# Kernel tuning notes

Hardware: AMD Instinct MI355X
Metric: run time of the kernel (lower is better)

Reference implementation:

```python
import jax, jax.numpy as jnp
import numpy as np

C_IN, K_R, K_C, N_K = 32, 3, 3, 64
STRIDE = (1, 1)
PAD = (1, 1)


def setup_inputs() -> dict:
    key = jax.random.key(0)
    k1, k2, k3 = jax.random.split(key, 3)
    x = jax.random.normal(k1, (32, C_IN, 128, 128), dtype=jnp.float32)
    kernels = jax.random.normal(k2, (N_K, K_R * K_C * C_IN), dtype=jnp.float32) * 0.05
    bias = jax.random.normal(k3, (N_K, 1), dtype=jnp.float32) * 0.05
    return {"x": x, "kernels": kernels, "bias": bias}


def reference(x, kernels, bias):
    # kernels rows are [C, kr, kc] flattened (per-channel im2col blocks stacked
    # along dim 0 in the original unroll) -> OIHW conv weight.
    w = kernels.reshape(N_K, C_IN, K_R, K_C)
    out = jax.lax.conv_general_dilated(
        x, w,
        window_strides=STRIDE,
        padding=[(PAD[0], PAD[0]), (PAD[1], PAD[1])],
        dimension_numbers=("NCHW", "OIHW", "NCHW"),
    )
    # bias (K, 1) broadcast over all output positions
    return out + bias.reshape(1, N_K, 1, 1)
```

## Files before the change

kernel.cpp:

```cpp
#include <hip/hip_runtime.h>
#include <hip/hip_bf16.h>


typedef __attribute__((ext_vector_type(8))) short bf16x8;
typedef __attribute__((ext_vector_type(4))) float f32x4;

#define NB 32
#define CIN 32
#define HH 128
#define WW 128
#define NK 64
#define XROW (130 * 32)

__device__ __forceinline__ unsigned short f2bf(float f) {
    union { float f; unsigned int u; } v; v.f = f;
    unsigned int u = v.u;
    return (unsigned short)((u + 0x7FFFu + ((u >> 16) & 1u)) >> 16);
}

__device__ __forceinline__ int xel(int wi, int c) {
    return wi * 32 + ((((c >> 3) ^ ((wi >> 2) & 3)) << 3) | (c & 7));
}

__global__ void repack_w(const float* __restrict__ kern,
                         unsigned short* __restrict__ wfrag) {
    int u = blockIdx.x * 256 + threadIdx.x;
    int j = u & 7;
    int lane = (u >> 3) & 63;
    int tile = (u >> 9) & 3;
    int kidx = u >> 11;
    int ok = tile * 16 + (lane & 15);
    int c = ((lane >> 4) << 3) + j;
    wfrag[u] = f2bf(kern[ok * 288 + c * 9 + kidx]);
}

__global__ __launch_bounds__(256, 4) void conv3x3_mfma(
        const float* __restrict__ x, const unsigned short* __restrict__ wfrag,
        const float* __restrict__ bias, float* __restrict__ out) {
    __shared__ unsigned short lds_x[3 * XROW];

    const int tid = threadIdx.x;
    const int bx = blockIdx.x;
    const int h = ((bx & 7) << 4) | (bx >> 3);
    const int n = blockIdx.y;
    const int lane = tid & 63;
    const int l16 = lane & 15;
    const int q = lane >> 4;
    const int wav = tid >> 6;
    const int ok_tile = (wav & 1) * 2;
    const int w_base = (wav >> 1) * 64;

    if (tid < 192) {
        int kr = tid >> 6;
        int idx = tid & 63;
        int c = idx & 31;
        int wi = (idx < 32) ? 0 : 129;
        lds_x[kr * XROW + xel(wi, c)] = 0;
    }

    #pragma unroll
    for (int kr = 0; kr < 3; ++kr) {
        const int r = h + kr - 1;
        const bool valid = (unsigned)r < HH;
        const float* xrow = x + ((size_t)(n * CIN) * HH + r) * WW;
        unsigned short* lrow = lds_x + kr * XROW;
        #pragma unroll
        for (int it = 0; it < 2; ++it) {
            int u = it * 256 + tid;
            int c = (u >> 5) * 2;
            int wq = u & 31;
            float4 va = {0.f, 0.f, 0.f, 0.f}, vb = {0.f, 0.f, 0.f, 0.f};
            if (valid) {
                va = *((const float4*)(xrow + (size_t)c * HH * WW) + wq);
                vb = *((const float4*)(xrow + (size_t)(c + 1) * HH * WW) + wq);
            }
            #pragma unroll
            for (int j = 0; j < 4; ++j) {
                int w = wq * 4 + j;
                __hip_bfloat162 h2 = __float22bfloat162_rn(
                    make_float2((&va.x)[j], (&vb.x)[j]));
                *(unsigned int*)&lrow[xel(w + 1, c)] = *(unsigned int*)&h2;
            }
        }
    }
    __syncthreads();

    f32x4 acc[2][4];
    #pragma unroll
    for (int mi = 0; mi < 2; ++mi)
        #pragma unroll
        for (int ni = 0; ni < 4; ++ni)
            acc[mi][ni] = (f32x4){0.f, 0.f, 0.f, 0.f};

    #pragma unroll 1
    for (int kr = 0; kr < 3; ++kr) {
        const unsigned short* lrow = lds_x + kr * XROW;
        #pragma unroll
        for (int kc = 0; kc < 3; ++kc) {
            const int kidx = kr * 3 + kc;
            bf16x8 afr[2];
            #pragma unroll
            for (int mi = 0; mi < 2; ++mi)
                afr[mi] = *(const bf16x8*)
                    &wfrag[(size_t)(((kidx * 4) + ok_tile + mi) * 64 + lane) * 8];
            #pragma unroll
            for (int ni = 0; ni < 4; ++ni) {
                bf16x8 bfr = *(const bf16x8*)&lrow[xel(w_base + ni * 16 + l16 + kc, q * 8)];
                #pragma unroll
                for (int mi = 0; mi < 2; ++mi)
                    acc[mi][ni] = __builtin_amdgcn_mfma_f32_16x16x32_bf16(
                        afr[mi], bfr, acc[mi][ni], 0, 0, 0);
            }
        }
    }

    #pragma unroll
    for (int mi = 0; mi < 2; ++mi) {
        #pragma unroll
        for (int rg = 0; rg < 4; ++rg) {
            int ok = (wav & 1) * 32 + mi * 16 + q * 4 + rg;
            float bv = bias[ok];
            float* orow = out + ((size_t)(n * NK + ok) * HH + h) * WW;
            #pragma unroll
            for (int ni = 0; ni < 4; ++ni)
                orow[w_base + ni * 16 + l16] = acc[mi][ni][rg] + bv;
        }
    }
}

extern "C" void kernel_launch(void* const* d_in, const int* in_sizes, int n_in,
                              void* d_out, int out_size, void* d_ws, size_t ws_size,
                              hipStream_t stream) {
    const float* x    = (const float*)d_in[0];
    const float* kern = (const float*)d_in[1];
    const float* bias = (const float*)d_in[2];
    float* out = (float*)d_out;
    unsigned short* wfrag = (unsigned short*)d_ws;

    repack_w<<<72, 256, 0, stream>>>(kern, wfrag);
    dim3 grid(HH, NB);
    conv3x3_mfma<<<grid, 256, 0, stream>>>(x, wfrag, bias, out);
}
```

Baseline: 197.7 us.

## Compute two output rows per block sharing a four-row LDS input tile

```diff
diff --git a/kernel.cpp b/kernel.cpp
--- a/kernel.cpp
+++ b/kernel.cpp
@@ -34,46 +34,47 @@
     wfrag[u] = f2bf(kern[ok * 288 + c * 9 + kidx]);
 }
 
-__global__ __launch_bounds__(256, 4) void conv3x3_mfma(
+__global__ __launch_bounds__(512, 6) void conv3x3_mfma(
         const float* __restrict__ x, const unsigned short* __restrict__ wfrag,
         const float* __restrict__ bias, float* __restrict__ out) {
-    __shared__ unsigned short lds_x[3 * XROW];
+    __shared__ unsigned short lds_x[4 * XROW];
 
     const int tid = threadIdx.x;
     const int bx = blockIdx.x;
-    const int h = ((bx & 7) << 4) | (bx >> 3);
+    const int hp = ((bx & 7) << 3) | (bx >> 3);
+    const int h0 = hp * 2;
     const int n = blockIdx.y;
     const int lane = tid & 63;
     const int l16 = lane & 15;
     const int q = lane >> 4;
     const int wav = tid >> 6;
-    const int ok_tile = (wav & 1) * 2;
-    const int w_base = (wav >> 1) * 64;
+    const int hsel = wav >> 2;
+    const int sub = wav & 3;
+    const int ok_tile = (sub & 1) * 2;
+    const int w_base = (sub >> 1) * 64;
 
-    if (tid < 192) {
-        int kr = tid >> 6;
+    if (tid < 256) {
+        int it = tid >> 6;
         int idx = tid & 63;
         int c = idx & 31;
         int wi = (idx < 32) ? 0 : 129;
-        lds_x[kr * XROW + xel(wi, c)] = 0;
+        lds_x[it * XROW + xel(wi, c)] = 0;
     }
 
-    #pragma unroll
-    for (int kr = 0; kr < 3; ++kr) {
-        const int r = h + kr - 1;
-        const bool valid = (unsigned)r < HH;
-        const float* xrow = x + ((size_t)(n * CIN) * HH + r) * WW;
-        unsigned short* lrow = lds_x + kr * XROW;
+    {
+        const int c = (tid >> 5) * 2;
+        const int wq = tid & 31;
         #pragma unroll
-        for (int it = 0; it < 2; ++it) {
-            int u = it * 256 + tid;
-            int c = (u >> 5) * 2;
-            int wq = u & 31;
+        for (int it = 0; it < 4; ++it) {
+            const int r = h0 - 1 + it;
+            const bool valid = (unsigned)r < HH;
             float4 va = {0.f, 0.f, 0.f, 0.f}, vb = {0.f, 0.f, 0.f, 0.f};
             if (valid) {
-                va = *((const float4*)(xrow + (size_t)c * HH * WW) + wq);
-                vb = *((const float4*)(xrow + (size_t)(c + 1) * HH * WW) + wq);
+                const float* xrow = x + (((size_t)n * CIN + c) * HH + r) * WW;
+                va = *((const float4*)xrow + wq);
+                vb = *((const float4*)(xrow + (size_t)HH * WW) + wq);
             }
+            unsigned short* lrow = lds_x + it * XROW;
             #pragma unroll
             for (int j = 0; j < 4; ++j) {
                 int w = wq * 4 + j;
@@ -94,7 +95,7 @@
 
     #pragma unroll 1
     for (int kr = 0; kr < 3; ++kr) {
-        const unsigned short* lrow = lds_x + kr * XROW;
+        const unsigned short* lrow = lds_x + (hsel + kr) * XROW;
         #pragma unroll
         for (int kc = 0; kc < 3; ++kc) {
             const int kidx = kr * 3 + kc;
@@ -114,13 +115,14 @@
         }
     }
 
+    const int h = h0 + hsel;
     #pragma unroll
     for (int mi = 0; mi < 2; ++mi) {
         #pragma unroll
         for (int rg = 0; rg < 4; ++rg) {
-            int ok = (wav & 1) * 32 + mi * 16 + q * 4 + rg;
+            int ok = (sub & 1) * 32 + mi * 16 + q * 4 + rg;
             float bv = bias[ok];
-            float* orow = out + ((size_t)(n * NK + ok) * HH + h) * WW;
+            float* orow = out + (((size_t)n * NK + ok) * HH + h) * WW;
             #pragma unroll
             for (int ni = 0; ni < 4; ++ni)
                 orow[w_base + ni * 16 + l16] = acc[mi][ni][rg] + bv;
@@ -138,6 +140,6 @@
     unsigned short* wfrag = (unsigned short*)d_ws;
 
     repack_w<<<72, 256, 0, stream>>>(kern, wfrag);
-    dim3 grid(HH, NB);
-    conv3x3_mfma<<<grid, 256, 0, stream>>>(x, wfrag, bias, out);
+    dim3 grid(64, NB);
+    conv3x3_mfma<<<grid, 512, 0, stream>>>(x, wfrag, bias, out);
 }
```

Result: no change. 199.6 us (+1.0%).
